# Kernel optimization log

Measured on AMD Instinct MI355X. Metric: run time of the kernel, lower is better.

Reference implementation:

```python
import jax, jax.numpy as jnp
import numpy as np

N_NODES = 100000
N_EDGES = 1200000
D = 64


def gcn_conv(x, src, dst, ew, W, b, n):
    # add self-loops with weight 1 (PyG GCNConv default)
    loops = jnp.arange(n)
    s = jnp.concatenate([src, loops])
    d = jnp.concatenate([dst, loops])
    w = jnp.concatenate([ew, jnp.ones((n,), ew.dtype)])
    deg = jax.ops.segment_sum(w, d, num_segments=n)           # [n]
    dis = jnp.where(deg > 0, jax.lax.rsqrt(deg), 0.0)
    norm = dis[s] * w * dis[d]                                # [E+n]
    h = x @ W                                                 # [n, out]
    msg = norm[:, None] * h[s]                                # gather
    out = jax.ops.segment_sum(msg, d, num_segments=n)         # scatter
    return out + b


def setup_inputs() -> dict:
    key = jax.random.key(0)
    ks = jax.random.split(key, 7)
    x = jax.random.normal(ks[0], (N_NODES, D), dtype=jnp.float32)
    edge_index = jax.random.randint(ks[1], (2, N_EDGES), 0, N_NODES, dtype=jnp.int64)
    edge_weight = jax.random.uniform(ks[2], (N_EDGES,), dtype=jnp.float32)
    W1 = jax.random.normal(ks[3], (D, D), dtype=jnp.float32) * (1.0 / np.sqrt(D))
    b1 = jnp.zeros((D,), dtype=jnp.float32)
    W2 = jax.random.normal(ks[4], (D, D), dtype=jnp.float32) * (1.0 / np.sqrt(D))
    b2 = jnp.zeros((D,), dtype=jnp.float32)
    return {"x": x, "edge_index": edge_index, "edge_weight": edge_weight,
            "W1": W1, "b1": b1, "W2": W2, "b2": b2}


def reference(x, edge_index, edge_weight, W1, b1, W2, b2):
    n = x.shape[0]
    src, dst = edge_index[0], edge_index[1]
    x1 = jax.nn.relu(gcn_conv(x, src, dst, edge_weight, W1, b1, n))
    x2 = jax.nn.relu(gcn_conv(x1, src, dst, edge_weight, W2, b2, n))
    return (x1 + x2) * 0.5
```

## Files before the change

kernel.cpp:

```cpp
#include <hip/hip_runtime.h>

#define NN 100000
#define NE 1200000
#define DD 64
#define NBUCK 196
#define BCAP 7168
#define TILE 4096
#define NB1 293
#define NB_G 1563
#define FIX25 33554432.0f
#define FIX25_INV (1.0f/33554432.0f)

typedef short bf16x8 __attribute__((ext_vector_type(8)));
typedef float f32x4  __attribute__((ext_vector_type(4)));

static __device__ __forceinline__ unsigned short f2bf(float f) {
    unsigned int u = __float_as_uint(f);
    unsigned int r = (u + 0x7fffu + ((u >> 16) & 1u)) >> 16;
    return (unsigned short)r;
}
static __device__ __forceinline__ float bf2f(unsigned short s) {
    return __uint_as_float(((unsigned int)s) << 16);
}


__global__ __launch_bounds__(256) void prep(
    int* __restrict__ cursor,
    const float* __restrict__ W1, const float* __restrict__ W2,
    unsigned short* __restrict__ Wt1, unsigned short* __restrict__ Wt2)
{
    if (blockIdx.x == 0) {
        if (threadIdx.x < NBUCK) cursor[threadIdx.x] = 0;
        return;
    }
    const float* W = (blockIdx.x == 1) ? W1 : W2;
    unsigned short* Wt = (blockIdx.x == 1) ? Wt1 : Wt2;
    int t = threadIdx.x;
    int col = t >> 2, k0 = (t & 3) * 16;
    #pragma unroll
    for (int i = 0; i < 16; ++i)
        Wt[col * 64 + k0 + i] = f2bf(W[(k0 + i) * 64 + col]);
}


static __device__ __forceinline__ void gemm_body(
    const float* __restrict__ x, const unsigned short* __restrict__ Wt,
    unsigned short* __restrict__ h16, int r0, int t,
    unsigned short* Xs, unsigned short* Ws)
{
    {
        int col = t >> 2, seg = (t & 3) * 16;
        const uint4* p = (const uint4*)(Wt + col * 64 + seg);
        uint4 a0 = p[0], a1 = p[1];
        *(uint4*)&Ws[col * 72 + seg]     = a0;
        *(uint4*)&Ws[col * 72 + seg + 8] = a1;
    }
    {
        int row = t >> 2, seg = (t & 3) * 16;
        int gr = r0 + row;
        float4 v0 = {0,0,0,0}, v1 = v0, v2 = v0, v3 = v0;
        if (gr < NN) {
            const float4* p = (const float4*)(x + (size_t)gr * DD + seg);
            v0 = p[0]; v1 = p[1]; v2 = p[2]; v3 = p[3];
        }
        ushort4 h0 = { f2bf(v0.x), f2bf(v0.y), f2bf(v0.z), f2bf(v0.w) };
        ushort4 h1 = { f2bf(v1.x), f2bf(v1.y), f2bf(v1.z), f2bf(v1.w) };
        ushort4 h2 = { f2bf(v2.x), f2bf(v2.y), f2bf(v2.z), f2bf(v2.w) };
        ushort4 h3 = { f2bf(v3.x), f2bf(v3.y), f2bf(v3.z), f2bf(v3.w) };
        *(ushort4*)&Xs[row * 72 + seg]      = h0;
        *(ushort4*)&Xs[row * 72 + seg + 4]  = h1;
        *(ushort4*)&Xs[row * 72 + seg + 8]  = h2;
        *(ushort4*)&Xs[row * 72 + seg + 12] = h3;
    }
    __syncthreads();

    const int wv = t >> 6;
    const int ln = t & 63;
    const int m  = ln & 15;
    const int q  = ln >> 4;
    const int arow = wv * 16 + m;

    bf16x8 a0 = *(const bf16x8*)&Xs[arow * 72 + q * 8];
    bf16x8 a1 = *(const bf16x8*)&Xs[arow * 72 + 32 + q * 8];

    f32x4 acc[4];
    #pragma unroll
    for (int c = 0; c < 4; ++c) {
        bf16x8 b0 = *(const bf16x8*)&Ws[(c * 16 + m) * 72 + q * 8];
        bf16x8 b1 = *(const bf16x8*)&Ws[(c * 16 + m) * 72 + 32 + q * 8];
        f32x4 z = {0.f, 0.f, 0.f, 0.f};
        z = __builtin_amdgcn_mfma_f32_16x16x32_bf16(a0, b0, z, 0, 0, 0);
        z = __builtin_amdgcn_mfma_f32_16x16x32_bf16(a1, b1, z, 0, 0, 0);
        acc[c] = z;
    }

    #pragma unroll
    for (int r = 0; r < 4; ++r) {
        int grow = r0 + wv * 16 + q * 4 + r;
        if (grow < NN) {
            #pragma unroll
            for (int c = 0; c < 4; ++c)
                h16[(size_t)grow * DD + c * 16 + m] = f2bf(acc[c][r]);
        }
    }
}


__global__ __launch_bounds__(256) void pass1_gemm(
    const int* __restrict__ src, const int* __restrict__ dst,
    const float* __restrict__ ew, int* __restrict__ cursor,
    unsigned long long* __restrict__ stage,
    const float* __restrict__ x, const unsigned short* __restrict__ Wt1,
    unsigned short* __restrict__ h16)
{
    __shared__ unsigned short Xs[64 * 72];
    __shared__ unsigned short Ws[64 * 72];
    __shared__ int cnt[NBUCK];
    __shared__ int resv[NBUCK];

    const int t = threadIdx.x;

    if (blockIdx.x >= NB1) {
        gemm_body(x, Wt1, h16, (blockIdx.x - NB1) * 64, t, Xs, Ws);
        return;
    }

    const int base = blockIdx.x * TILE;
    if (t < NBUCK) cnt[t] = 0;
    __syncthreads();

    #pragma unroll
    for (int k = 0; k < TILE / 256; ++k) {
        int e = base + k * 256 + t;
        if (e < NE) atomicAdd(&cnt[dst[e] >> 9], 1);
    }
    __syncthreads();
    if (t < NBUCK) {
        int c = cnt[t];
        resv[t] = c ? atomicAdd(&cursor[t], c) : 0;
        cnt[t] = 0;
    }
    __syncthreads();
    #pragma unroll
    for (int k = 0; k < TILE / 256; ++k) {
        int e = base + k * 256 + t;
        if (e < NE) {
            int d = dst[e];
            int b = d >> 9;
            int r = atomicAdd(&cnt[b], 1);
            int pos = resv[b] + r;
            if (pos < BCAP) {
                unsigned int meta = ((unsigned int)(d & 511) << 17) |
                                    (unsigned int)src[e];
                stage[(size_t)b * BCAP + pos] =
                    ((unsigned long long)meta << 32) | __float_as_uint(ew[e]);
            }
        }
    }
}


__global__ __launch_bounds__(512) void pass2(
    const unsigned long long* __restrict__ stage, const int* __restrict__ cursor,
    unsigned int* __restrict__ csr, unsigned int* __restrict__ rowdeg,
    float* __restrict__ dis)
{
    __shared__ unsigned long long sb[BCAP];
    __shared__ int cnt[512];
    __shared__ unsigned sum[512];
    __shared__ int lptr[512];

    const int b = blockIdx.x;
    const int t = threadIdx.x;
    const int n0 = b << 9;
    const int cntb = min(cursor[b], BCAP);

    cnt[t] = 0; sum[t] = 0;
    __syncthreads();

    for (int k = t; k < cntb; k += 512) {
        unsigned long long E = stage[(size_t)b * BCAP + k];
        unsigned int meta = (unsigned int)(E >> 32);
        int dl = meta >> 17;
        float w = __uint_as_float((unsigned int)E);
        int r = atomicAdd(&cnt[dl], 1);
        atomicAdd(&sum[dl], (unsigned)(w * FIX25));
        unsigned int meta2 = ((unsigned int)dl << 23) |
                             ((unsigned int)min(r, 63) << 17) |
                             (meta & 0x1ffffu);
        sb[k] = ((unsigned long long)meta2 << 32) |
                ((r < 64) ? (unsigned long long)f2bf(w) : 0xffffffffull);
    }
    __syncthreads();

    int v = cnt[t];
    __syncthreads();
    for (int off = 1; off < 512; off <<= 1) {
        int add = (t >= off) ? cnt[t - off] : 0;
        __syncthreads();
        cnt[t] += add;
        __syncthreads();
    }
    lptr[t] = cnt[t] - v;

    int node = n0 + t;
    if (node < NN) {
        float deg = 1.0f + (float)sum[t] * FIX25_INV;
        dis[node] = rsqrtf(deg);
        rowdeg[node] = ((unsigned)(b * BCAP + (cnt[t] - v)) << 6) |
                       (unsigned)min(v, 63);
    }
    __syncthreads();

    for (int k = t; k < cntb; k += 512) {
        unsigned long long E = sb[k];
        if ((unsigned int)E == 0xffffffffu) continue;
        unsigned int meta2 = (unsigned int)(E >> 32);
        int dl = meta2 >> 23;
        int r  = (meta2 >> 17) & 63;
        unsigned int s = meta2 & 0x1ffffu;
        csr[b * BCAP + lptr[dl] + r] =
            (s << 15) | ((unsigned int)E & 0x7fffu);
    }
}


__global__ __launch_bounds__(256) void bake(
    unsigned int* __restrict__ csr, const int* __restrict__ cursor,
    const float* __restrict__ dis)
{
    const int b  = blockIdx.x / 7;
    const int k0 = (blockIdx.x % 7) * 1024;
    const int cntb = min(cursor[b], BCAP);
    const int kend = min(k0 + 1024, cntb);
    for (int k = k0 + threadIdx.x; k < kend; k += 256) {
        unsigned int e = csr[b * BCAP + k];
        unsigned int s = e >> 15;
        float nm = dis[s] * bf2f((unsigned short)(e & 0x7fffu));
        csr[b * BCAP + k] = (e & 0xffff8000u) | (f2bf(nm) & 0x7fffu);
    }
}


template <bool FINAL>
__global__ __launch_bounds__(256) void gather(
    const unsigned short* __restrict__ h16, const float* __restrict__ bias,
    const float* __restrict__ dis, const unsigned int* __restrict__ rowdeg,
    const unsigned int* __restrict__ csr,
    const float* __restrict__ prev, float* __restrict__ out)
{
    const int node = __builtin_amdgcn_readfirstlane(
        (blockIdx.x * blockDim.x + threadIdx.x) >> 6);
    const int lane = threadIdx.x & 63;
    if (node >= NN) return;

    const unsigned int rd = rowdeg[node];
    const int deg = rd & 63;
    const float di = dis[node];

    float a0 = fmaf(di * di, bf2f(h16[node * DD + lane]), bias[lane]);
    float a1 = 0.f, a2 = 0.f, a3 = 0.f;

    const unsigned int* seg = csr + (rd >> 6);
    int j = 0;
    for (; j + 3 < deg; j += 4) {
        unsigned int e0 = seg[j],     e1 = seg[j + 1];
        unsigned int e2 = seg[j + 2], e3 = seg[j + 3];
        float n0 = bf2f((unsigned short)(e0 & 0x7fffu)) * di;
        float n1 = bf2f((unsigned short)(e1 & 0x7fffu)) * di;
        float n2 = bf2f((unsigned short)(e2 & 0x7fffu)) * di;
        float n3 = bf2f((unsigned short)(e3 & 0x7fffu)) * di;
        a0 = fmaf(n0, bf2f(h16[(e0 >> 15) * DD + lane]), a0);
        a1 = fmaf(n1, bf2f(h16[(e1 >> 15) * DD + lane]), a1);
        a2 = fmaf(n2, bf2f(h16[(e2 >> 15) * DD + lane]), a2);
        a3 = fmaf(n3, bf2f(h16[(e3 >> 15) * DD + lane]), a3);
    }
    for (; j < deg; ++j) {
        unsigned int e = seg[j];
        a0 = fmaf(bf2f((unsigned short)(e & 0x7fffu)) * di,
                  bf2f(h16[(e >> 15) * DD + lane]), a0);
    }

    float v = fmaxf((a0 + a1) + (a2 + a3), 0.f);
    int idx = node * DD + lane;
    if (FINAL) out[idx] = 0.5f * (prev[idx] + v);
    else       out[idx] = v;
}

__global__ __launch_bounds__(256) void gemm_mfma(
    const float* __restrict__ x, const unsigned short* __restrict__ Wt,
    unsigned short* __restrict__ h16)
{
    __shared__ unsigned short Xs[64 * 72];
    __shared__ unsigned short Ws[64 * 72];
    gemm_body(x, Wt, h16, blockIdx.x * 64, threadIdx.x, Xs, Ws);
}


extern "C" void kernel_launch(void* const* d_in, const int* in_sizes, int n_in,
                              void* d_out, int out_size, void* d_ws, size_t ws_size,
                              hipStream_t stream) {
    const float* x   = (const float*)d_in[0];
    const int*   ei  = (const int*)d_in[1];
    const float* ewt = (const float*)d_in[2];
    const float* W1  = (const float*)d_in[3];
    const float* b1  = (const float*)d_in[4];
    const float* W2  = (const float*)d_in[5];
    const float* b2  = (const float*)d_in[6];
    float* out = (float*)d_out;

    const int* srcv = ei;
    const int* dstv = ei + NE;

    float* wsf = (float*)d_ws;
    int* cursor = (int*)wsf;
    unsigned short* Wt1 = (unsigned short*)(wsf + 256);
    unsigned short* Wt2 = Wt1 + 4096;
    float* dis = wsf + 4352;
    unsigned int* rowdeg = (unsigned int*)(wsf + 104448);
    unsigned long long* stage = (unsigned long long*)(wsf + 204544);
    unsigned int* csr = (unsigned int*)(wsf + 204544 + 2 * NBUCK * BCAP);
    unsigned short* h16 = (unsigned short*)(csr + NBUCK * BCAP);

    const int GB = (NN * 64) / 256;

    prep<<<3, 256, 0, stream>>>(cursor, W1, W2, Wt1, Wt2);
    pass1_gemm<<<NB1 + NB_G, 256, 0, stream>>>(srcv, dstv, ewt, cursor, stage,
                                               x, Wt1, h16);
    pass2<<<NBUCK, 512, 0, stream>>>(stage, cursor, csr, rowdeg, dis);
    bake<<<NBUCK * 7, 256, 0, stream>>>(csr, cursor, dis);

    gather<false><<<GB, 256, 0, stream>>>(h16, b1, dis, rowdeg, csr, nullptr, out);
    gemm_mfma<<<NB_G, 256, 0, stream>>>(out, Wt2, h16);
    gather<true><<<GB, 256, 0, stream>>>(h16, b2, dis, rowdeg, csr, out, out);
}
```

Measured before the change: 222.4 us.

## Split wave into four edge groups with vectorized ushort4 feature gathers

The gather kernel now splits each 64-lane wave into four 16-lane groups. Each group handles a different edge and loads four bf16 features per lane as a ushort4, instead of every lane loading one feature for the same edge. Partial sums are combined across groups with xor shuffles, and one group writes the result as float4. The aim is wider loads and more edges in flight per wave. In exchange, the padded 16-edge iterations do wasted work on low-degree nodes and the shuffle reduction adds cost.

```diff
diff --git a/kernel.cpp b/kernel.cpp
--- a/kernel.cpp
+++ b/kernel.cpp
@@ -254,37 +254,79 @@
     const int lane = threadIdx.x & 63;
     if (node >= NN) return;
 
+    const int g = lane >> 4;
+    const int l = lane & 15;
+    const int l4 = l << 2;
+
     const unsigned int rd = rowdeg[node];
     const int deg = rd & 63;
     const float di = dis[node];
-
-    float a0 = fmaf(di * di, bf2f(h16[node * DD + lane]), bias[lane]);
-    float a1 = 0.f, a2 = 0.f, a3 = 0.f;
-
     const unsigned int* seg = csr + (rd >> 6);
-    int j = 0;
-    for (; j + 3 < deg; j += 4) {
-        unsigned int e0 = seg[j],     e1 = seg[j + 1];
-        unsigned int e2 = seg[j + 2], e3 = seg[j + 3];
-        float n0 = bf2f((unsigned short)(e0 & 0x7fffu)) * di;
-        float n1 = bf2f((unsigned short)(e1 & 0x7fffu)) * di;
-        float n2 = bf2f((unsigned short)(e2 & 0x7fffu)) * di;
-        float n3 = bf2f((unsigned short)(e3 & 0x7fffu)) * di;
-        a0 = fmaf(n0, bf2f(h16[(e0 >> 15) * DD + lane]), a0);
-        a1 = fmaf(n1, bf2f(h16[(e1 >> 15) * DD + lane]), a1);
-        a2 = fmaf(n2, bf2f(h16[(e2 >> 15) * DD + lane]), a2);
-        a3 = fmaf(n3, bf2f(h16[(e3 >> 15) * DD + lane]), a3);
-    }
-    for (; j < deg; ++j) {
-        unsigned int e = seg[j];
-        a0 = fmaf(bf2f((unsigned short)(e & 0x7fffu)) * di,
-                  bf2f(h16[(e >> 15) * DD + lane]), a0);
-    }
-
-    float v = fmaxf((a0 + a1) + (a2 + a3), 0.f);
-    int idx = node * DD + lane;
-    if (FINAL) out[idx] = 0.5f * (prev[idx] + v);
-    else       out[idx] = v;
+
+    const ushort4 hs = *(const ushort4*)(h16 + (size_t)node * DD + l4);
+    const float4  bb = *(const float4*)(bias + l4);
+    float4 p = {0.f, 0.f, 0.f, 0.f};
+    if (FINAL) p = *(const float4*)(prev + (size_t)node * DD + l4);
+
+    f32x4 acc0 = {0,0,0,0}, acc1 = {0,0,0,0}, acc2 = {0,0,0,0}, acc3 = {0,0,0,0};
+
+#define QUAD(q, rq, nq)                                                        \
+    {                                                                          \
+        unsigned w0 = seg[j + 4*q + 0], w1 = seg[j + 4*q + 1];                 \
+        unsigned w2 = seg[j + 4*q + 2], w3 = seg[j + 4*q + 3];                 \
+        unsigned ea = (g & 1) ? w1 : w0;                                       \
+        unsigned eb = (g & 1) ? w3 : w2;                                       \
+        unsigned e  = (g & 2) ? eb : ea;                                       \
+        e = ((j + 4*q + g) < deg) ? e : 0u;                                    \
+        nq = bf2f((unsigned short)(e & 0x7fffu)) * di;                         \
+        rq = *(const ushort4*)(h16 + ((size_t)(e >> 15) << 6) + l4);           \
+    }
+#define FMA4(rq, nq, ac)                                                       \
+    ac[0] = fmaf(nq, bf2f(rq.x), ac[0]);                                       \
+    ac[1] = fmaf(nq, bf2f(rq.y), ac[1]);                                       \
+    ac[2] = fmaf(nq, bf2f(rq.z), ac[2]);                                       \
+    ac[3] = fmaf(nq, bf2f(rq.w), ac[3]);
+
+    for (int j = 0; j < deg; j += 16) {
+        ushort4 r0, r1, r2, r3;
+        float n0, n1, n2, n3;
+        QUAD(0, r0, n0)
+        QUAD(1, r1, n1)
+        QUAD(2, r2, n2)
+        QUAD(3, r3, n3)
+        FMA4(r0, n0, acc0)
+        FMA4(r1, n1, acc1)
+        FMA4(r2, n2, acc2)
+        FMA4(r3, n3, acc3)
+    }
+#undef QUAD
+#undef FMA4
+
+    float s0 = (acc0[0] + acc1[0]) + (acc2[0] + acc3[0]);
+    float s1 = (acc0[1] + acc1[1]) + (acc2[1] + acc3[1]);
+    float s2 = (acc0[2] + acc1[2]) + (acc2[2] + acc3[2]);
+    float s3 = (acc0[3] + acc1[3]) + (acc2[3] + acc3[3]);
+
+    s0 += __shfl_xor(s0, 16); s1 += __shfl_xor(s1, 16);
+    s2 += __shfl_xor(s2, 16); s3 += __shfl_xor(s3, 16);
+    s0 += __shfl_xor(s0, 32); s1 += __shfl_xor(s1, 32);
+    s2 += __shfl_xor(s2, 32); s3 += __shfl_xor(s3, 32);
+
+    if (g == 0) {
+        const float dd = di * di;
+        float v0 = fmaxf(fmaf(dd, bf2f(hs.x), bb.x) + s0, 0.f);
+        float v1 = fmaxf(fmaf(dd, bf2f(hs.y), bb.y) + s1, 0.f);
+        float v2 = fmaxf(fmaf(dd, bf2f(hs.z), bb.z) + s2, 0.f);
+        float v3 = fmaxf(fmaf(dd, bf2f(hs.w), bb.w) + s3, 0.f);
+        float4 o;
+        if (FINAL) {
+            o.x = 0.5f * (p.x + v0); o.y = 0.5f * (p.y + v1);
+            o.z = 0.5f * (p.z + v2); o.w = 0.5f * (p.w + v3);
+        } else {
+            o.x = v0; o.y = v1; o.z = v2; o.w = v3;
+        }
+        *(float4*)(out + (size_t)node * DD + l4) = o;
+    }
 }
 
 __global__ __launch_bounds__(256) void gemm_mfma(
```

New measurement: 209.0 us. 6.1% less time.
